# Kernel optimization log

Hardware: AMD Instinct MI355X
Metric: run time of the kernel (lower is better)

## Reference

```python
import jax, jax.numpy as jnp
import numpy as np
import math

# ---- model dimensions (match init_kwargs / input_specs) ----
B, LQ, LK = 2, 1024, 1024          # batch, q_dim (query seq len), kv_dim (key seq len)
D_HEAD, H = 64, 16                 # head_size = d_model // n_heads, n_heads
D_MODEL = D_HEAD * H               # 1024
C_FACTOR = 5
U_SEL  = int(C_FACTOR * math.log(LQ))   # u  = 34 selected (top) queries
U_SAMP = int(LQ * math.log(LK))         # U  = 7097 randomly sampled keys


def setup_inputs() -> dict:
    key = jax.random.key(0)
    kq, kk, kv, kw, kb = jax.random.split(key, 5)
    q = jax.random.normal(kq, (B, LQ, D_HEAD), dtype=jnp.float32)
    k = jax.random.normal(kk, (B, LK, D_HEAD), dtype=jnp.float32)
    v = jax.random.normal(kv, (B, LK, D_HEAD), dtype=jnp.float32)
    # final projection Linear(n_heads*head_size, d_model), stored as (in, out)
    W_proj = jax.random.normal(kw, (D_MODEL, D_MODEL), dtype=jnp.float32) * 0.02
    b_proj = jax.random.normal(kb, (D_MODEL,), dtype=jnp.float32) * 0.02
    return {"q": q, "k": k, "v": v, "W_proj": W_proj, "b_proj": b_proj}


def _probsparse_head(head_key, q, k, v):
    """One ProbSparse head: q,k,v are (B, L, D_HEAD). Returns (B, LQ, D_HEAD)."""
    b_idx = jnp.arange(B)[:, None]
    # _sampler: per-batch random key indices, shape (B, U_SAMP)
    idx = jax.random.randint(head_key, (B, U_SAMP), 0, LK)
    k_bar = k[b_idx, idx]                                   # (B, U_SAMP, D)
    # sparsity measure M = max - mean over sampled scores
    s_bar = jnp.einsum('bqd,bud->bqu', q, k_bar)            # (B, LQ, U_SAMP)
    M = s_bar.max(axis=-1) - s_bar.mean(axis=-1)            # (B, LQ)
    _, top_idx = jax.lax.top_k(M, U_SEL)                    # (B, U_SEL)
    q_bar = q[b_idx, top_idx]                               # (B, U_SEL, D)
    # attention on the selected queries only; scale = sqrt(kv seq len) as in source
    attn = jnp.einsum('bud,bkd->buk', q_bar, k) / jnp.sqrt(jnp.float32(LK))
    attn = jax.nn.softmax(attn, axis=-1)
    s1 = jnp.einsum('buk,bkd->bud', attn, v)                # (B, U_SEL, D)
    # non-selected rows get mean(v); selected rows get attention output
    s = jnp.broadcast_to(v.mean(axis=1, keepdims=True), (B, LQ, D_HEAD))
    return s.at[b_idx, top_idx].set(s1)


def reference(q, k, v, W_proj, b_proj):
    # heads share q,k,v; differ only in random key sampling -> map sequentially over head keys
    head_keys = jax.random.split(jax.random.key(42), H)
    heads = jax.lax.map(lambda hk: _probsparse_head(hk, q, k, v), head_keys)  # (H,B,LQ,D)
    # concat along feature dim == transpose + reshape
    attn_out = jnp.transpose(heads, (1, 2, 0, 3)).reshape(B, LQ, H * D_HEAD)
    return attn_out @ W_proj + b_proj                        # (B, LQ, D_MODEL)
```

## Files before the change

### kernel.cpp

```cpp
#include <hip/hip_runtime.h>
#include <math.h>
#include <stdint.h>
#include <stddef.h>


#define BB     2
#define LQ     1024
#define LK     1024
#define DH     64
#define NH     16
#define DM     1024
#define USEL   34
#define USAMP  7097
#define NSLICE 8
#define NJ     8
#define JS     (LK / NJ)

#define THREEFRY_PARTITIONABLE 1

__device__ __forceinline__ uint32_t rotl32(uint32_t x, int d) {
  return (x << d) | (x >> (32 - d));
}

__device__ __forceinline__ void threefry2x32(uint32_t k0, uint32_t k1,
                                             uint32_t x0, uint32_t x1,
                                             uint32_t& o0, uint32_t& o1) {
  uint32_t ks2 = k0 ^ k1 ^ 0x1BD11BDAu;
  x0 += k0; x1 += k1;
#define TFR(r) { x0 += x1; x1 = rotl32(x1, (r)); x1 ^= x0; }
  TFR(13) TFR(15) TFR(26) TFR(6)
  x0 += k1; x1 += ks2 + 1u;
  TFR(17) TFR(29) TFR(16) TFR(24)
  x0 += ks2; x1 += k0 + 2u;
  TFR(13) TFR(15) TFR(26) TFR(6)
  x0 += k0; x1 += k1 + 3u;
  TFR(17) TFR(29) TFR(16) TFR(24)
  x0 += k1; x1 += ks2 + 4u;
  TFR(13) TFR(15) TFR(26) TFR(6)
  x0 += ks2; x1 += k0 + 5u;
#undef TFR
  o0 = x0; o1 = x1;
}

__global__ void k_zero(unsigned* __restrict__ p, int n) {
  int i = blockIdx.x * blockDim.x + threadIdx.x;
  if (i < n) p[i] = 0u;
}

__global__ void k_sample(unsigned* __restrict__ counts) {
  __shared__ uint32_t sk[2];
  int h = blockIdx.y;
  if (threadIdx.x == 0) {
    uint32_t hk0, hk1, t0, t1;
#if THREEFRY_PARTITIONABLE
    threefry2x32(0u, 42u, 0u, (uint32_t)h, hk0, hk1);
    threefry2x32(hk0, hk1, 0u, 1u, t0, t1);
    sk[0] = t0; sk[1] = t1;
#else
    uint32_t a0, a1, b0, b1, c0, c1;
    int i0 = 2 * h, i1 = 2 * h + 1;
    if (i0 < 16) { threefry2x32(0u, 42u, (uint32_t)i0, (uint32_t)(i0 + 16), a0, a1); hk0 = a0; }
    else         { threefry2x32(0u, 42u, (uint32_t)(i0 - 16), (uint32_t)i0, a0, a1); hk0 = a1; }
    if (i1 < 16) { threefry2x32(0u, 42u, (uint32_t)i1, (uint32_t)(i1 + 16), a0, a1); hk1 = a0; }
    else         { threefry2x32(0u, 42u, (uint32_t)(i1 - 16), (uint32_t)i1, a0, a1); hk1 = a1; }
    threefry2x32(hk0, hk1, 0u, 2u, b0, b1);
    threefry2x32(hk0, hk1, 1u, 3u, c0, c1);
    sk[0] = b1; sk[1] = c1;
#endif
  }
  __syncthreads();
  int j = blockIdx.x * blockDim.x + threadIdx.x;
  if (j >= USAMP) return;
  for (int b = 0; b < BB; b++) {
    uint32_t o0, o1, bits;
#if THREEFRY_PARTITIONABLE
    threefry2x32(sk[0], sk[1], 0u, (uint32_t)(b * USAMP + j), o0, o1);
    bits = o0 ^ o1;
#else
    threefry2x32(sk[0], sk[1], (uint32_t)j, (uint32_t)(j + USAMP), o0, o1);
    bits = (b == 0) ? o0 : o1;
#endif
    atomicAdd(&counts[((size_t)h * BB + b) * LK + (bits & (LK - 1))], 1u);
  }
}

__global__ __launch_bounds__(256) void k_means(const float* __restrict__ kk,
                                               const float* __restrict__ v,
                                               const unsigned* __restrict__ counts,
                                               float* __restrict__ kmean,
                                               float* __restrict__ vmean) {
  int task = blockIdx.y, s = blockIdx.x, t = threadIdx.x;
  int d4 = t & 15, jsub = t >> 4;
  __shared__ float4 part[16][16];
  float4 acc = make_float4(0.f, 0.f, 0.f, 0.f);
  if (task < NH * BB) {
    int b = task & 1;
    const unsigned* cnt = counts + (size_t)task * LK;
    const float4* kb4 = (const float4*)(kk + (size_t)b * LK * DH);
#pragma unroll
    for (int jj = 0; jj < LK / (16 * NSLICE); jj++) {
      int j = s * (LK / NSLICE) + jsub + 16 * jj;
      float c = (float)cnt[j];
      float4 kv = kb4[j * 16 + d4];
      acc.x += c * kv.x; acc.y += c * kv.y; acc.z += c * kv.z; acc.w += c * kv.w;
    }
  } else {
    int b = task - NH * BB;
    const float4* vb4 = (const float4*)(v + (size_t)b * LK * DH);
#pragma unroll
    for (int jj = 0; jj < LK / (16 * NSLICE); jj++) {
      int j = s * (LK / NSLICE) + jsub + 16 * jj;
      float4 kv = vb4[j * 16 + d4];
      acc.x += kv.x; acc.y += kv.y; acc.z += kv.z; acc.w += kv.w;
    }
  }
  part[jsub][d4] = acc;
  __syncthreads();
  if (t < 16) {
    float4 sum = part[0][t];
#pragma unroll
    for (int x = 1; x < 16; x++) {
      float4 p = part[x][t];
      sum.x += p.x; sum.y += p.y; sum.z += p.z; sum.w += p.w;
    }
    float scale = (task < NH * BB) ? (1.0f / (float)USAMP) : (1.0f / (float)LK);
    float* dst = (task < NH * BB) ? (kmean + (size_t)task * DH)
                                  : (vmean + (size_t)(task - NH * BB) * DH);
    atomicAdd(&dst[t * 4 + 0], sum.x * scale);
    atomicAdd(&dst[t * 4 + 1], sum.y * scale);
    atomicAdd(&dst[t * 4 + 2], sum.z * scale);
    atomicAdd(&dst[t * 4 + 3], sum.w * scale);
  }
}

__global__ __launch_bounds__(256) void k_scores(const float* __restrict__ q,
                                                const float* __restrict__ k,
                                                float* __restrict__ S) {
  __shared__ float Qt[DH][68];
  __shared__ float Kt[DH][68];
  int b = blockIdx.z;
  int i0 = blockIdx.y * 64, j0 = blockIdx.x * 64;
  int t = threadIdx.x;
  const float* qb = q + ((size_t)b * LQ + i0) * DH;
  const float* kb = k + ((size_t)b * LK + j0) * DH;
#pragma unroll
  for (int rep = 0; rep < 4; rep++) {
    int lin = (rep * 256 + t) * 4;
    int r = lin >> 6, c = lin & 63;
    float4 qv = *(const float4*)(qb + (size_t)r * DH + c);
    float4 kv = *(const float4*)(kb + (size_t)r * DH + c);
    Qt[c][r] = qv.x; Qt[c + 1][r] = qv.y; Qt[c + 2][r] = qv.z; Qt[c + 3][r] = qv.w;
    Kt[c][r] = kv.x; Kt[c + 1][r] = kv.y; Kt[c + 2][r] = kv.z; Kt[c + 3][r] = kv.w;
  }
  __syncthreads();
  int tx = t & 15, ty = t >> 4;
  float acc[4][4] = {};
#pragma unroll 8
  for (int d = 0; d < DH; d++) {
    float4 av = *(const float4*)&Qt[d][ty * 4];
    float4 bv = *(const float4*)&Kt[d][tx * 4];
    acc[0][0] += av.x * bv.x; acc[0][1] += av.x * bv.y; acc[0][2] += av.x * bv.z; acc[0][3] += av.x * bv.w;
    acc[1][0] += av.y * bv.x; acc[1][1] += av.y * bv.y; acc[1][2] += av.y * bv.z; acc[1][3] += av.y * bv.w;
    acc[2][0] += av.z * bv.x; acc[2][1] += av.z * bv.y; acc[2][2] += av.z * bv.z; acc[2][3] += av.z * bv.w;
    acc[3][0] += av.w * bv.x; acc[3][1] += av.w * bv.y; acc[3][2] += av.w * bv.z; acc[3][3] += av.w * bv.w;
  }
  float* Sb = S + ((size_t)b * LQ + i0) * LK + j0;
#pragma unroll
  for (int r = 0; r < 4; r++) {
    *(float4*)(Sb + (size_t)(ty * 4 + r) * LK + tx * 4) =
        make_float4(acc[r][0], acc[r][1], acc[r][2], acc[r][3]);
  }
}

__global__ __launch_bounds__(256) void k_M(const float* __restrict__ q,
                                           const float* __restrict__ S,
                                           const unsigned* __restrict__ counts,
                                           const float* __restrict__ kmean,
                                           float* __restrict__ M) {
  int b = blockIdx.y;
  __shared__ uint32_t mask[NH][LK / 32];
  int t = threadIdx.x;
  for (int w = t; w < NH * (LK / 32); w += 256) {
    int h = w >> 5, blk = w & 31;
    const unsigned* cnt = counts + ((size_t)h * BB + b) * LK + blk * 32;
    uint32_t m = 0;
    for (int z = 0; z < 32; z++) m |= (cnt[z] != 0u ? 1u : 0u) << z;
    mask[h][blk] = m;
  }
  __syncthreads();
  int lane = t & 63, w4 = t >> 6;
  int i = blockIdx.x * 4 + w4;
  const float* Srow = S + ((size_t)b * LQ + i) * LK;
  float mx[NH];
#pragma unroll
  for (int h = 0; h < NH; h++) mx[h] = -INFINITY;
  for (int j = lane; j < LK; j += 64) {
    float s = Srow[j];
#pragma unroll
    for (int h = 0; h < NH; h++) {
      bool on = (mask[h][j >> 5] >> (j & 31)) & 1u;
      mx[h] = fmaxf(mx[h], on ? s : -INFINITY);
    }
  }
#pragma unroll
  for (int h = 0; h < NH; h++) {
#pragma unroll
    for (int off = 32; off > 0; off >>= 1) mx[h] = fmaxf(mx[h], __shfl_xor(mx[h], off));
  }
  float qv = q[((size_t)b * LQ + i) * DH + lane];
#pragma unroll
  for (int h = 0; h < NH; h++) {
    float p = qv * kmean[((size_t)h * BB + b) * DH + lane];
#pragma unroll
    for (int off = 32; off > 0; off >>= 1) p += __shfl_xor(p, off);
    mx[h] -= p;
  }
  if (lane == 0) {
#pragma unroll
    for (int h = 0; h < NH; h++) M[((size_t)h * BB + b) * LQ + i] = mx[h];
  }
}

__global__ __launch_bounds__(256) void k_topk(const float* __restrict__ M,
                                              int* __restrict__ topidx) {
  int hb = blockIdx.x, t = threadIdx.x;
  __shared__ float vals[LQ];
  __shared__ float wv[4];
  __shared__ int   wi[4];
  for (int i = t; i < LQ; i += 256) vals[i] = M[(size_t)hb * LQ + i];
  __syncthreads();
  int lane = t & 63, w = t >> 6;
  for (int u = 0; u < USEL; u++) {
    float bv = -INFINITY; int bi = 0x7fffffff;
#pragma unroll
    for (int r = 0; r < 4; r++) {
      int i = r * 256 + t;
      float x = vals[i];
      if (x > bv) { bv = x; bi = i; }
    }
#pragma unroll
    for (int off = 32; off > 0; off >>= 1) {
      float ov = __shfl_xor(bv, off);
      int   oi = __shfl_xor(bi, off);
      if (ov > bv || (ov == bv && oi < bi)) { bv = ov; bi = oi; }
    }
    if (lane == 0) { wv[w] = bv; wi[w] = bi; }
    __syncthreads();
    if (t == 0) {
      float fv = wv[0]; int fi = wi[0];
#pragma unroll
      for (int x = 1; x < 4; x++)
        if (wv[x] > fv || (wv[x] == fv && wi[x] < fi)) { fv = wv[x]; fi = wi[x]; }
      topidx[hb * USEL + u] = fi;
      vals[fi] = -INFINITY;
    }
    __syncthreads();
  }
}

__global__ __launch_bounds__(256) void k_smax(const float* __restrict__ S,
                                              const int* __restrict__ topidx,
                                              float* __restrict__ smax,
                                              float* __restrict__ ssum) {
  int hb = blockIdx.y, u = blockIdx.x, b = hb & 1;
  int t = threadIdx.x, lane = t & 63, w = t >> 6;
  __shared__ float wred[4], wred2[4];
  int i = topidx[hb * USEL + u];
  const float* Srow = S + ((size_t)b * LQ + i) * LK;
  float x[4], lmx = -INFINITY;
#pragma unroll
  for (int r = 0; r < 4; r++) {
    x[r] = Srow[r * 256 + t] * 0.03125f;
    lmx = fmaxf(lmx, x[r]);
  }
#pragma unroll
  for (int off = 32; off > 0; off >>= 1) lmx = fmaxf(lmx, __shfl_xor(lmx, off));
  if (lane == 0) wred[w] = lmx;
  __syncthreads();
  float mx = fmaxf(fmaxf(wred[0], wred[1]), fmaxf(wred[2], wred[3]));
  float ls = expf(x[0] - mx) + expf(x[1] - mx) + expf(x[2] - mx) + expf(x[3] - mx);
#pragma unroll
  for (int off = 32; off > 0; off >>= 1) ls += __shfl_xor(ls, off);
  if (lane == 0) wred2[w] = ls;
  __syncthreads();
  if (t == 0) {
    smax[hb * USEL + u] = mx;
    ssum[hb * USEL + u] = wred2[0] + wred2[1] + wred2[2] + wred2[3];
  }
}

__global__ __launch_bounds__(256) void k_pv(const float* __restrict__ S,
                                            const float* __restrict__ v,
                                            const int* __restrict__ topidx,
                                            const float* __restrict__ smax,
                                            float* __restrict__ delta_raw) {
  int hb = blockIdx.y, s = blockIdx.x, b = hb & 1;
  int t = threadIdx.x, d = t & 63, g = t >> 6;
  __shared__ float p[USEL][JS];
  __shared__ float part[4][USEL][DH];
  for (int idx = t; idx < USEL * JS; idx += 256) {
    int u = idx >> 7, jj = idx & (JS - 1);
    int i = topidx[hb * USEL + u];
    float xs = S[((size_t)b * LQ + i) * LK + s * JS + jj];
    p[u][jj] = expf(xs * 0.03125f - smax[hb * USEL + u]);
  }
  __syncthreads();
  float vreg[32];
  const float* vb = v + ((size_t)b * LK + s * JS + g * 32) * DH + d;
#pragma unroll
  for (int jj = 0; jj < 32; jj++) vreg[jj] = vb[(size_t)jj * DH];
  for (int u = 0; u < USEL; u++) {
    float acc = 0.f;
#pragma unroll
    for (int j4 = 0; j4 < 8; j4++) {
      float4 pp = *(const float4*)&p[u][g * 32 + j4 * 4];
      acc += pp.x * vreg[j4 * 4] + pp.y * vreg[j4 * 4 + 1] +
             pp.z * vreg[j4 * 4 + 2] + pp.w * vreg[j4 * 4 + 3];
    }
    part[g][u][d] = acc;
  }
  __syncthreads();
  for (int idx = t; idx < USEL * DH; idx += 256) {
    int u = idx >> 6, dd = idx & 63;
    float sum = part[0][u][dd] + part[1][u][dd] + part[2][u][dd] + part[3][u][dd];
    atomicAdd(&delta_raw[((size_t)hb * USEL + u) * DH + dd], sum);
  }
}

__global__ __launch_bounds__(256) void k_base(const float* __restrict__ W,
                                              const float* __restrict__ vmean,
                                              float* __restrict__ base) {
  __shared__ float vm[DH];
  int b = blockIdx.y, hc = blockIdx.z;
  int o = blockIdx.x * 256 + threadIdx.x;
  if (threadIdx.x < DH) vm[threadIdx.x] = vmean[b * DH + threadIdx.x];
  __syncthreads();
  const float* Wr = W + (size_t)hc * DH * DM + o;
  float acc = 0.f;
#pragma unroll
  for (int d = 0; d < DH; d++) acc += vm[d] * Wr[(size_t)d * DM];
  atomicAdd(&base[b * DM + o], acc);
}

__global__ __launch_bounds__(256) void k_fill(const float* __restrict__ base,
                                              const float* __restrict__ bproj,
                                              float* __restrict__ out) {
  int idx = blockIdx.x * 256 + threadIdx.x;
  int o4 = idx & (DM / 4 - 1);
  int b = idx >> 18;
  float4 bs = ((const float4*)base)[b * (DM / 4) + o4];
  float4 bp = ((const float4*)bproj)[o4];
  ((float4*)out)[idx] = make_float4(bs.x + bp.x, bs.y + bp.y, bs.z + bp.z, bs.w + bp.w);
}

__global__ __launch_bounds__(256) void k_corr(const float* __restrict__ W,
                                              const int* __restrict__ topidx,
                                              const float* __restrict__ delta_raw,
                                              const float* __restrict__ ssum,
                                              const float* __restrict__ vmean,
                                              float* __restrict__ out) {
  int u = blockIdx.x, hb = blockIdx.y;
  int h = hb >> 1, b = hb & 1;
  int t = threadIdx.x;
  __shared__ float dl[DH];
  int i = topidx[hb * USEL + u];
  if (t < DH) {
    float inv = 1.0f / ssum[hb * USEL + u];
    dl[t] = delta_raw[((size_t)hb * USEL + u) * DH + t] * inv - vmean[b * DH + t];
  }
  __syncthreads();
  const float* Wh = W + (size_t)h * DH * DM;
  float* orow = out + ((size_t)b * LQ + i) * DM;
#pragma unroll
  for (int rep = 0; rep < 4; rep++) {
    int o = rep * 256 + t;
    float acc = 0.f;
#pragma unroll 16
    for (int d = 0; d < DH; d++) acc += dl[d] * Wh[(size_t)d * DM + o];
    atomicAdd(&orow[o], acc);
  }
}

extern "C" void kernel_launch(void* const* d_in, const int* in_sizes, int n_in,
                              void* d_out, int out_size, void* d_ws, size_t ws_size,
                              hipStream_t stream) {
  const float* q  = (const float*)d_in[0];
  const float* k  = (const float*)d_in[1];
  const float* v  = (const float*)d_in[2];
  const float* W  = (const float*)d_in[3];
  const float* bp = (const float*)d_in[4];
  float* out = (float*)d_out;

  float* S = out;

  char* w = (char*)d_ws;
  unsigned* counts    = (unsigned*)w;         w += (size_t)NH * BB * LK * 4;
  float*    base      = (float*)w;            w += (size_t)BB * DM * 4;
  float*    kmean     = (float*)w;            w += (size_t)NH * BB * DH * 4;
  float*    vmean     = (float*)w;            w += (size_t)BB * DH * 4;
  float*    delta_raw = (float*)w;            w += (size_t)NH * BB * USEL * DH * 4;
  float*    M         = (float*)w;            w += (size_t)NH * BB * LQ * 4;
  int*      topidx    = (int*)w;              w += (size_t)NH * BB * USEL * 4;
  float*    smax      = (float*)w;            w += (size_t)NH * BB * USEL * 4;
  float*    ssum      = (float*)w;            w += (size_t)NH * BB * USEL * 4;
  if ((size_t)(w - (char*)d_ws) > ws_size) return;

  const int ZW = NH * BB * LK + BB * DM + NH * BB * DH + BB * DH + NH * BB * USEL * DH;
  k_zero  <<<(ZW + 255) / 256, 256, 0, stream>>>(counts, ZW);
  k_sample<<<dim3((USAMP + 255) / 256, NH), 256, 0, stream>>>(counts);
  k_means <<<dim3(NSLICE, NH * BB + BB), 256, 0, stream>>>(k, v, counts, kmean, vmean);
  k_scores<<<dim3(LK / 64, LQ / 64, BB), 256, 0, stream>>>(q, k, S);
  k_M     <<<dim3(LQ / 4, BB), 256, 0, stream>>>(q, S, counts, kmean, M);
  k_topk  <<<NH * BB, 256, 0, stream>>>(M, topidx);
  k_smax  <<<dim3(USEL, NH * BB), 256, 0, stream>>>(S, topidx, smax, ssum);
  k_pv    <<<dim3(NJ, NH * BB), 256, 0, stream>>>(S, v, topidx, smax, delta_raw);
  k_base  <<<dim3(DM / 256, BB, NH), 256, 0, stream>>>(W, vmean, base);
  k_fill  <<<(BB * LQ * DM / 4) / 256, 256, 0, stream>>>(base, bp, out);
  k_corr  <<<dim3(USEL, NH * BB), 256, 0, stream>>>(W, topidx, delta_raw, ssum, vmean, out);
}
```

Baseline: 177.0 us.

## Drop softmax max pass, fold row sums into PV kernel, single-wave top-k

Removes the k_smax kernel by computing softmax numerators without max subtraction and accumulating the row sums atomically inside k_pv. Rewrites top-k as a single 64-lane wave holding its values in registers, which removes the shared-memory round trips and block barriers on each of the 34 iterations. This saves one kernel launch and one read of the selected score rows. The cost is no max-shift in the exponent, which relies on the 1/32-scaled scores staying small enough not to overflow, plus extra atomics on ssum.

```diff
diff --git a/kernel.cpp b/kernel.cpp
--- a/kernel.cpp
+++ b/kernel.cpp
@@ -221,21 +221,19 @@
   }
 }
 
-__global__ __launch_bounds__(256) void k_topk(const float* __restrict__ M,
-                                              int* __restrict__ topidx) {
-  int hb = blockIdx.x, t = threadIdx.x;
-  __shared__ float vals[LQ];
-  __shared__ float wv[4];
-  __shared__ int   wi[4];
-  for (int i = t; i < LQ; i += 256) vals[i] = M[(size_t)hb * LQ + i];
-  __syncthreads();
-  int lane = t & 63, w = t >> 6;
+__global__ __launch_bounds__(64) void k_topk(const float* __restrict__ M,
+                                             int* __restrict__ topidx) {
+  int hb = blockIdx.x, lane = threadIdx.x;
+  const float* Mh = M + (size_t)hb * LQ;
+  float r[16];
+#pragma unroll
+  for (int c = 0; c < 16; c++) r[c] = Mh[c * 64 + lane];
   for (int u = 0; u < USEL; u++) {
     float bv = -INFINITY; int bi = 0x7fffffff;
 #pragma unroll
-    for (int r = 0; r < 4; r++) {
-      int i = r * 256 + t;
-      float x = vals[i];
+    for (int c = 0; c < 16; c++) {
+      float x = r[c];
+      int i = c * 64 + lane;
       if (x > bv) { bv = x; bi = i; }
     }
 #pragma unroll
@@ -244,56 +242,19 @@
       int   oi = __shfl_xor(bi, off);
       if (ov > bv || (ov == bv && oi < bi)) { bv = ov; bi = oi; }
     }
-    if (lane == 0) { wv[w] = bv; wi[w] = bi; }
-    __syncthreads();
-    if (t == 0) {
-      float fv = wv[0]; int fi = wi[0];
-#pragma unroll
-      for (int x = 1; x < 4; x++)
-        if (wv[x] > fv || (wv[x] == fv && wi[x] < fi)) { fv = wv[x]; fi = wi[x]; }
-      topidx[hb * USEL + u] = fi;
-      vals[fi] = -INFINITY;
-    }
-    __syncthreads();
-  }
-}
-
-__global__ __launch_bounds__(256) void k_smax(const float* __restrict__ S,
-                                              const int* __restrict__ topidx,
-                                              float* __restrict__ smax,
-                                              float* __restrict__ ssum) {
-  int hb = blockIdx.y, u = blockIdx.x, b = hb & 1;
-  int t = threadIdx.x, lane = t & 63, w = t >> 6;
-  __shared__ float wred[4], wred2[4];
-  int i = topidx[hb * USEL + u];
-  const float* Srow = S + ((size_t)b * LQ + i) * LK;
-  float x[4], lmx = -INFINITY;
-#pragma unroll
-  for (int r = 0; r < 4; r++) {
-    x[r] = Srow[r * 256 + t] * 0.03125f;
-    lmx = fmaxf(lmx, x[r]);
-  }
-#pragma unroll
-  for (int off = 32; off > 0; off >>= 1) lmx = fmaxf(lmx, __shfl_xor(lmx, off));
-  if (lane == 0) wred[w] = lmx;
-  __syncthreads();
-  float mx = fmaxf(fmaxf(wred[0], wred[1]), fmaxf(wred[2], wred[3]));
-  float ls = expf(x[0] - mx) + expf(x[1] - mx) + expf(x[2] - mx) + expf(x[3] - mx);
-#pragma unroll
-  for (int off = 32; off > 0; off >>= 1) ls += __shfl_xor(ls, off);
-  if (lane == 0) wred2[w] = ls;
-  __syncthreads();
-  if (t == 0) {
-    smax[hb * USEL + u] = mx;
-    ssum[hb * USEL + u] = wred2[0] + wred2[1] + wred2[2] + wred2[3];
+    if (lane == 0) topidx[hb * USEL + u] = bi;
+    int wc = bi >> 6, wl = bi & 63;
+#pragma unroll
+    for (int c = 0; c < 16; c++)
+      if (c == wc && lane == wl) r[c] = -INFINITY;
   }
 }
 
 __global__ __launch_bounds__(256) void k_pv(const float* __restrict__ S,
                                             const float* __restrict__ v,
                                             const int* __restrict__ topidx,
-                                            const float* __restrict__ smax,
-                                            float* __restrict__ delta_raw) {
+                                            float* __restrict__ delta_raw,
+                                            float* __restrict__ ssum) {
   int hb = blockIdx.y, s = blockIdx.x, b = hb & 1;
   int t = threadIdx.x, d = t & 63, g = t >> 6;
   __shared__ float p[USEL][JS];
@@ -302,7 +263,7 @@
     int u = idx >> 7, jj = idx & (JS - 1);
     int i = topidx[hb * USEL + u];
     float xs = S[((size_t)b * LQ + i) * LK + s * JS + jj];
-    p[u][jj] = expf(xs * 0.03125f - smax[hb * USEL + u]);
+    p[u][jj] = expf(xs * 0.03125f);
   }
   __syncthreads();
   float vreg[32];
@@ -318,6 +279,13 @@
              pp.z * vreg[j4 * 4 + 2] + pp.w * vreg[j4 * 4 + 3];
     }
     part[g][u][d] = acc;
+  }
+  if (t < USEL * 4) {
+    int u = t >> 2, ch = t & 3;
+    float sum = 0.f;
+#pragma unroll
+    for (int jj = 0; jj < 32; jj++) sum += p[u][ch * 32 + jj];
+    atomicAdd(&ssum[hb * USEL + u], sum);
   }
   __syncthreads();
   for (int idx = t; idx < USEL * DH; idx += 256) {
@@ -399,21 +367,20 @@
   float*    kmean     = (float*)w;            w += (size_t)NH * BB * DH * 4;
   float*    vmean     = (float*)w;            w += (size_t)BB * DH * 4;
   float*    delta_raw = (float*)w;            w += (size_t)NH * BB * USEL * DH * 4;
+  float*    ssum      = (float*)w;            w += (size_t)NH * BB * USEL * 4;
   float*    M         = (float*)w;            w += (size_t)NH * BB * LQ * 4;
   int*      topidx    = (int*)w;              w += (size_t)NH * BB * USEL * 4;
-  float*    smax      = (float*)w;            w += (size_t)NH * BB * USEL * 4;
-  float*    ssum      = (float*)w;            w += (size_t)NH * BB * USEL * 4;
   if ((size_t)(w - (char*)d_ws) > ws_size) return;
 
-  const int ZW = NH * BB * LK + BB * DM + NH * BB * DH + BB * DH + NH * BB * USEL * DH;
+  const int ZW = NH * BB * LK + BB * DM + NH * BB * DH + BB * DH +
+                 NH * BB * USEL * DH + NH * BB * USEL;
   k_zero  <<<(ZW + 255) / 256, 256, 0, stream>>>(counts, ZW);
   k_sample<<<dim3((USAMP + 255) / 256, NH), 256, 0, stream>>>(counts);
   k_means <<<dim3(NSLICE, NH * BB + BB), 256, 0, stream>>>(k, v, counts, kmean, vmean);
   k_scores<<<dim3(LK / 64, LQ / 64, BB), 256, 0, stream>>>(q, k, S);
   k_M     <<<dim3(LQ / 4, BB), 256, 0, stream>>>(q, S, counts, kmean, M);
-  k_topk  <<<NH * BB, 256, 0, stream>>>(M, topidx);
-  k_smax  <<<dim3(USEL, NH * BB), 256, 0, stream>>>(S, topidx, smax, ssum);
-  k_pv    <<<dim3(NJ, NH * BB), 256, 0, stream>>>(S, v, topidx, smax, delta_raw);
+  k_topk  <<<NH * BB, 64, 0, stream>>>(M, topidx);
+  k_pv    <<<dim3(NJ, NH * BB), 256, 0, stream>>>(S, v, topidx, delta_raw, ssum);
   k_base  <<<dim3(DM / 256, BB, NH), 256, 0, stream>>>(W, vmean, base);
   k_fill  <<<(BB * LQ * DM / 4) / 256, 256, 0, stream>>>(base, bp, out);
   k_corr  <<<dim3(USEL, NH * BB), 256, 0, stream>>>(W, topidx, delta_raw, ssum, vmean, out);
```

Result: slower. 184.8 us (+4.4%).

## Remove zero and softmax-max kernels by using shared-memory histograms and partial buffers

Applied to the files above, without the earlier changes.

The sampling kernel now builds each per-(head,batch) key histogram in shared memory and writes it out directly. The global atomics, which needed a separate zeroing kernel, are replaced by per-slice partial buffers that the consumer kernels sum. The separate softmax max/sum kernel is removed: k_pv computes unshifted exp values and partial sums, relying on the small scaled score range. This cuts two kernel launches and many global atomics, but drops the max-subtraction safeguard and makes k_fill read 16 partial base rows per output element.

```diff
diff --git a/kernel.cpp b/kernel.cpp
--- a/kernel.cpp
+++ b/kernel.cpp
@@ -42,53 +42,52 @@
   o0 = x0; o1 = x1;
 }
 
-__global__ void k_zero(unsigned* __restrict__ p, int n) {
-  int i = blockIdx.x * blockDim.x + threadIdx.x;
-  if (i < n) p[i] = 0u;
-}
-
-__global__ void k_sample(unsigned* __restrict__ counts) {
-  __shared__ uint32_t sk[2];
-  int h = blockIdx.y;
-  if (threadIdx.x == 0) {
-    uint32_t hk0, hk1, t0, t1;
+__global__ __launch_bounds__(1024) void k_sample(unsigned* __restrict__ counts) {
+  int hb = blockIdx.x, h = hb >> 1, b = hb & 1;
+  int t = threadIdx.x;
+  __shared__ unsigned hist[LK];
+  hist[t] = 0u;
+  uint32_t sk0, sk1;
 #if THREEFRY_PARTITIONABLE
+  {
+    uint32_t hk0, hk1;
     threefry2x32(0u, 42u, 0u, (uint32_t)h, hk0, hk1);
-    threefry2x32(hk0, hk1, 0u, 1u, t0, t1);
-    sk[0] = t0; sk[1] = t1;
+    threefry2x32(hk0, hk1, 0u, 1u, sk0, sk1);
+  }
 #else
-    uint32_t a0, a1, b0, b1, c0, c1;
+  {
+    uint32_t hk0, hk1, a0, a1, b0_, b1_, c0_, c1_;
     int i0 = 2 * h, i1 = 2 * h + 1;
     if (i0 < 16) { threefry2x32(0u, 42u, (uint32_t)i0, (uint32_t)(i0 + 16), a0, a1); hk0 = a0; }
     else         { threefry2x32(0u, 42u, (uint32_t)(i0 - 16), (uint32_t)i0, a0, a1); hk0 = a1; }
     if (i1 < 16) { threefry2x32(0u, 42u, (uint32_t)i1, (uint32_t)(i1 + 16), a0, a1); hk1 = a0; }
     else         { threefry2x32(0u, 42u, (uint32_t)(i1 - 16), (uint32_t)i1, a0, a1); hk1 = a1; }
-    threefry2x32(hk0, hk1, 0u, 2u, b0, b1);
-    threefry2x32(hk0, hk1, 1u, 3u, c0, c1);
-    sk[0] = b1; sk[1] = c1;
+    threefry2x32(hk0, hk1, 0u, 2u, b0_, b1_);
+    threefry2x32(hk0, hk1, 1u, 3u, c0_, c1_);
+    sk0 = b1_; sk1 = c1_;
+  }
 #endif
-  }
-  __syncthreads();
-  int j = blockIdx.x * blockDim.x + threadIdx.x;
-  if (j >= USAMP) return;
-  for (int b = 0; b < BB; b++) {
+  __syncthreads();
+  for (int j = t; j < USAMP; j += 1024) {
     uint32_t o0, o1, bits;
 #if THREEFRY_PARTITIONABLE
-    threefry2x32(sk[0], sk[1], 0u, (uint32_t)(b * USAMP + j), o0, o1);
+    threefry2x32(sk0, sk1, 0u, (uint32_t)(b * USAMP + j), o0, o1);
     bits = o0 ^ o1;
 #else
-    threefry2x32(sk[0], sk[1], (uint32_t)j, (uint32_t)(j + USAMP), o0, o1);
+    threefry2x32(sk0, sk1, (uint32_t)j, (uint32_t)(j + USAMP), o0, o1);
     bits = (b == 0) ? o0 : o1;
 #endif
-    atomicAdd(&counts[((size_t)h * BB + b) * LK + (bits & (LK - 1))], 1u);
-  }
+    atomicAdd(&hist[bits & (LK - 1)], 1u);
+  }
+  __syncthreads();
+  counts[(size_t)hb * LK + t] = hist[t];
 }
 
 __global__ __launch_bounds__(256) void k_means(const float* __restrict__ kk,
                                                const float* __restrict__ v,
                                                const unsigned* __restrict__ counts,
-                                               float* __restrict__ kmean,
-                                               float* __restrict__ vmean) {
+                                               float* __restrict__ kmean_part,
+                                               float* __restrict__ vmean_part) {
   int task = blockIdx.y, s = blockIdx.x, t = threadIdx.x;
   int d4 = t & 15, jsub = t >> 4;
   __shared__ float4 part[16][16];
@@ -123,13 +122,17 @@
       float4 p = part[x][t];
       sum.x += p.x; sum.y += p.y; sum.z += p.z; sum.w += p.w;
     }
-    float scale = (task < NH * BB) ? (1.0f / (float)USAMP) : (1.0f / (float)LK);
-    float* dst = (task < NH * BB) ? (kmean + (size_t)task * DH)
-                                  : (vmean + (size_t)(task - NH * BB) * DH);
-    atomicAdd(&dst[t * 4 + 0], sum.x * scale);
-    atomicAdd(&dst[t * 4 + 1], sum.y * scale);
-    atomicAdd(&dst[t * 4 + 2], sum.z * scale);
-    atomicAdd(&dst[t * 4 + 3], sum.w * scale);
+    if (task < NH * BB) {
+      float* dst = kmean_part + ((size_t)s * NH * BB + task) * DH;
+      const float sc = 1.0f / (float)USAMP;
+      dst[t * 4 + 0] = sum.x * sc; dst[t * 4 + 1] = sum.y * sc;
+      dst[t * 4 + 2] = sum.z * sc; dst[t * 4 + 3] = sum.w * sc;
+    } else {
+      float* dst = vmean_part + ((size_t)s * BB + (task - NH * BB)) * DH;
+      const float sc = 1.0f / (float)LK;
+      dst[t * 4 + 0] = sum.x * sc; dst[t * 4 + 1] = sum.y * sc;
+      dst[t * 4 + 2] = sum.z * sc; dst[t * 4 + 3] = sum.w * sc;
+    }
   }
 }
 
@@ -175,10 +178,11 @@
 __global__ __launch_bounds__(256) void k_M(const float* __restrict__ q,
                                            const float* __restrict__ S,
                                            const unsigned* __restrict__ counts,
-                                           const float* __restrict__ kmean,
+                                           const float* __restrict__ kmean_part,
                                            float* __restrict__ M) {
   int b = blockIdx.y;
   __shared__ uint32_t mask[NH][LK / 32];
+  __shared__ float kmean_s[NH][DH];
   int t = threadIdx.x;
   for (int w = t; w < NH * (LK / 32); w += 256) {
     int h = w >> 5, blk = w & 31;
@@ -187,6 +191,14 @@
     for (int z = 0; z < 32; z++) m |= (cnt[z] != 0u ? 1u : 0u) << z;
     mask[h][blk] = m;
   }
+  for (int idx = t; idx < NH * DH; idx += 256) {
+    int h = idx >> 6, d = idx & 63;
+    float sum = 0.f;
+#pragma unroll
+    for (int sl = 0; sl < NSLICE; sl++)
+      sum += kmean_part[((size_t)sl * NH * BB + h * BB + b) * DH + d];
+    kmean_s[h][d] = sum;
+  }
   __syncthreads();
   int lane = t & 63, w4 = t >> 6;
   int i = blockIdx.x * 4 + w4;
@@ -210,7 +222,7 @@
   float qv = q[((size_t)b * LQ + i) * DH + lane];
 #pragma unroll
   for (int h = 0; h < NH; h++) {
-    float p = qv * kmean[((size_t)h * BB + b) * DH + lane];
+    float p = qv * kmean_s[h][lane];
 #pragma unroll
     for (int off = 32; off > 0; off >>= 1) p += __shfl_xor(p, off);
     mx[h] -= p;
@@ -258,42 +270,11 @@
   }
 }
 
-__global__ __launch_bounds__(256) void k_smax(const float* __restrict__ S,
-                                              const int* __restrict__ topidx,
-                                              float* __restrict__ smax,
-                                              float* __restrict__ ssum) {
-  int hb = blockIdx.y, u = blockIdx.x, b = hb & 1;
-  int t = threadIdx.x, lane = t & 63, w = t >> 6;
-  __shared__ float wred[4], wred2[4];
-  int i = topidx[hb * USEL + u];
-  const float* Srow = S + ((size_t)b * LQ + i) * LK;
-  float x[4], lmx = -INFINITY;
-#pragma unroll
-  for (int r = 0; r < 4; r++) {
-    x[r] = Srow[r * 256 + t] * 0.03125f;
-    lmx = fmaxf(lmx, x[r]);
-  }
-#pragma unroll
-  for (int off = 32; off > 0; off >>= 1) lmx = fmaxf(lmx, __shfl_xor(lmx, off));
-  if (lane == 0) wred[w] = lmx;
-  __syncthreads();
-  float mx = fmaxf(fmaxf(wred[0], wred[1]), fmaxf(wred[2], wred[3]));
-  float ls = expf(x[0] - mx) + expf(x[1] - mx) + expf(x[2] - mx) + expf(x[3] - mx);
-#pragma unroll
-  for (int off = 32; off > 0; off >>= 1) ls += __shfl_xor(ls, off);
-  if (lane == 0) wred2[w] = ls;
-  __syncthreads();
-  if (t == 0) {
-    smax[hb * USEL + u] = mx;
-    ssum[hb * USEL + u] = wred2[0] + wred2[1] + wred2[2] + wred2[3];
-  }
-}
-
 __global__ __launch_bounds__(256) void k_pv(const float* __restrict__ S,
                                             const float* __restrict__ v,
                                             const int* __restrict__ topidx,
-                                            const float* __restrict__ smax,
-                                            float* __restrict__ delta_raw) {
+                                            float* __restrict__ delta_part,
+                                            float* __restrict__ ssum_part) {
   int hb = blockIdx.y, s = blockIdx.x, b = hb & 1;
   int t = threadIdx.x, d = t & 63, g = t >> 6;
   __shared__ float p[USEL][JS];
@@ -302,7 +283,7 @@
     int u = idx >> 7, jj = idx & (JS - 1);
     int i = topidx[hb * USEL + u];
     float xs = S[((size_t)b * LQ + i) * LK + s * JS + jj];
-    p[u][jj] = expf(xs * 0.03125f - smax[hb * USEL + u]);
+    p[u][jj] = expf(xs * 0.03125f);
   }
   __syncthreads();
   float vreg[32];
@@ -319,45 +300,62 @@
     }
     part[g][u][d] = acc;
   }
+  if (t < USEL * 4) {
+    int u = t >> 2, ch = t & 3;
+    float sum = 0.f;
+#pragma unroll
+    for (int jj = 0; jj < 32; jj++) sum += p[u][ch * 32 + jj];
+    ssum_part[(((size_t)s * NH * BB + hb) * USEL + u) * 4 + ch] = sum;
+  }
   __syncthreads();
   for (int idx = t; idx < USEL * DH; idx += 256) {
     int u = idx >> 6, dd = idx & 63;
     float sum = part[0][u][dd] + part[1][u][dd] + part[2][u][dd] + part[3][u][dd];
-    atomicAdd(&delta_raw[((size_t)hb * USEL + u) * DH + dd], sum);
+    delta_part[(((size_t)s * NH * BB + hb) * USEL + u) * DH + dd] = sum;
   }
 }
 
 __global__ __launch_bounds__(256) void k_base(const float* __restrict__ W,
-                                              const float* __restrict__ vmean,
-                                              float* __restrict__ base) {
+                                              const float* __restrict__ vmean_part,
+                                              float* __restrict__ base_part) {
   __shared__ float vm[DH];
   int b = blockIdx.y, hc = blockIdx.z;
   int o = blockIdx.x * 256 + threadIdx.x;
-  if (threadIdx.x < DH) vm[threadIdx.x] = vmean[b * DH + threadIdx.x];
+  if (threadIdx.x < DH) {
+    float s = 0.f;
+#pragma unroll
+    for (int sl = 0; sl < NSLICE; sl++)
+      s += vmean_part[((size_t)sl * BB + b) * DH + threadIdx.x];
+    vm[threadIdx.x] = s;
+  }
   __syncthreads();
   const float* Wr = W + (size_t)hc * DH * DM + o;
   float acc = 0.f;
 #pragma unroll
   for (int d = 0; d < DH; d++) acc += vm[d] * Wr[(size_t)d * DM];
-  atomicAdd(&base[b * DM + o], acc);
-}
-
-__global__ __launch_bounds__(256) void k_fill(const float* __restrict__ base,
+  base_part[((size_t)hc * BB + b) * DM + o] = acc;
+}
+
+__global__ __launch_bounds__(256) void k_fill(const float* __restrict__ base_part,
                                               const float* __restrict__ bproj,
                                               float* __restrict__ out) {
   int idx = blockIdx.x * 256 + threadIdx.x;
   int o4 = idx & (DM / 4 - 1);
-  int b = idx >> 18;
-  float4 bs = ((const float4*)base)[b * (DM / 4) + o4];
-  float4 bp = ((const float4*)bproj)[o4];
-  ((float4*)out)[idx] = make_float4(bs.x + bp.x, bs.y + bp.y, bs.z + bp.z, bs.w + bp.w);
+  int b = (idx >> 18) & 1;
+  float4 bs = ((const float4*)bproj)[o4];
+#pragma unroll
+  for (int hc = 0; hc < NH; hc++) {
+    float4 p = ((const float4*)base_part)[((size_t)hc * BB + b) * (DM / 4) + o4];
+    bs.x += p.x; bs.y += p.y; bs.z += p.z; bs.w += p.w;
+  }
+  ((float4*)out)[idx] = bs;
 }
 
 __global__ __launch_bounds__(256) void k_corr(const float* __restrict__ W,
                                               const int* __restrict__ topidx,
-                                              const float* __restrict__ delta_raw,
-                                              const float* __restrict__ ssum,
-                                              const float* __restrict__ vmean,
+                                              const float* __restrict__ delta_part,
+                                              const float* __restrict__ ssum_part,
+                                              const float* __restrict__ vmean_part,
                                               float* __restrict__ out) {
   int u = blockIdx.x, hb = blockIdx.y;
   int h = hb >> 1, b = hb & 1;
@@ -365,8 +363,17 @@
   __shared__ float dl[DH];
   int i = topidx[hb * USEL + u];
   if (t < DH) {
-    float inv = 1.0f / ssum[hb * USEL + u];
-    dl[t] = delta_raw[((size_t)hb * USEL + u) * DH + t] * inv - vmean[b * DH + t];
+    float ss = 0.f, dr = 0.f, vm = 0.f;
+#pragma unroll
+    for (int sl = 0; sl < NJ; sl++) {
+      const float* sp = ssum_part + (((size_t)sl * NH * BB + hb) * USEL + u) * 4;
+      ss += sp[0] + sp[1] + sp[2] + sp[3];
+      dr += delta_part[(((size_t)sl * NH * BB + hb) * USEL + u) * DH + t];
+    }
+#pragma unroll
+    for (int sl = 0; sl < NSLICE; sl++)
+      vm += vmean_part[((size_t)sl * BB + b) * DH + t];
+    dl[t] = dr / ss - vm;
   }
   __syncthreads();
   const float* Wh = W + (size_t)h * DH * DM;
@@ -394,27 +401,23 @@
   float* S = out;
 
   char* w = (char*)d_ws;
-  unsigned* counts    = (unsigned*)w;         w += (size_t)NH * BB * LK * 4;
-  float*    base      = (float*)w;            w += (size_t)BB * DM * 4;
-  float*    kmean     = (float*)w;            w += (size_t)NH * BB * DH * 4;
-  float*    vmean     = (float*)w;            w += (size_t)BB * DH * 4;
-  float*    delta_raw = (float*)w;            w += (size_t)NH * BB * USEL * DH * 4;
-  float*    M         = (float*)w;            w += (size_t)NH * BB * LQ * 4;
-  int*      topidx    = (int*)w;              w += (size_t)NH * BB * USEL * 4;
-  float*    smax      = (float*)w;            w += (size_t)NH * BB * USEL * 4;
-  float*    ssum      = (float*)w;            w += (size_t)NH * BB * USEL * 4;
+  unsigned* counts     = (unsigned*)w;  w += (size_t)NH * BB * LK * 4;
+  float*    kmean_part = (float*)w;     w += (size_t)NSLICE * NH * BB * DH * 4;
+  float*    vmean_part = (float*)w;     w += (size_t)NSLICE * BB * DH * 4;
+  float*    base_part  = (float*)w;     w += (size_t)NH * BB * DM * 4;
+  float*    delta_part = (float*)w;     w += (size_t)NJ * NH * BB * USEL * DH * 4;
+  float*    ssum_part  = (float*)w;     w += (size_t)NJ * NH * BB * USEL * 4 * 4;
+  float*    M          = (float*)w;     w += (size_t)NH * BB * LQ * 4;
+  int*      topidx     = (int*)w;       w += (size_t)NH * BB * USEL * 4;
   if ((size_t)(w - (char*)d_ws) > ws_size) return;
 
-  const int ZW = NH * BB * LK + BB * DM + NH * BB * DH + BB * DH + NH * BB * USEL * DH;
-  k_zero  <<<(ZW + 255) / 256, 256, 0, stream>>>(counts, ZW);
-  k_sample<<<dim3((USAMP + 255) / 256, NH), 256, 0, stream>>>(counts);
-  k_means <<<dim3(NSLICE, NH * BB + BB), 256, 0, stream>>>(k, v, counts, kmean, vmean);
+  k_sample<<<NH * BB, 1024, 0, stream>>>(counts);
+  k_means <<<dim3(NSLICE, NH * BB + BB), 256, 0, stream>>>(k, v, counts, kmean_part, vmean_part);
   k_scores<<<dim3(LK / 64, LQ / 64, BB), 256, 0, stream>>>(q, k, S);
-  k_M     <<<dim3(LQ / 4, BB), 256, 0, stream>>>(q, S, counts, kmean, M);
+  k_M     <<<dim3(LQ / 4, BB), 256, 0, stream>>>(q, S, counts, kmean_part, M);
   k_topk  <<<NH * BB, 256, 0, stream>>>(M, topidx);
-  k_smax  <<<dim3(USEL, NH * BB), 256, 0, stream>>>(S, topidx, smax, ssum);
-  k_pv    <<<dim3(NJ, NH * BB), 256, 0, stream>>>(S, v, topidx, smax, delta_raw);
-  k_base  <<<dim3(DM / 256, BB, NH), 256, 0, stream>>>(W, vmean, base);
-  k_fill  <<<(BB * LQ * DM / 4) / 256, 256, 0, stream>>>(base, bp, out);
-  k_corr  <<<dim3(USEL, NH * BB), 256, 0, stream>>>(W, topidx, delta_raw, ssum, vmean, out);
-}
+  k_pv    <<<dim3(NJ, NH * BB), 256, 0, stream>>>(S, v, topidx, delta_part, ssum_part);
+  k_base  <<<dim3(DM / 256, BB, NH), 256, 0, stream>>>(W, vmean_part, base_part);
+  k_fill  <<<(BB * LQ * DM / 4) / 256, 256, 0, stream>>>(base_part, bp, out);
+  k_corr  <<<dim3(USEL, NH * BB), 256, 0, stream>>>(W, topidx, delta_part, ssum_part, vmean_part, out);
+}
```

Result: no change. 178.2 us (+0.7%).
